# Performance work log

Measured on AMD Instinct MI355X. Metric: run time of the kernel, lower is better.

## Reference

```python
import jax, jax.numpy as jnp
import numpy as np

EPS = 1e-8
COMMITMENT_COST = 0.25
NUM_EMBEDDINGS = 8192
EMBEDDING_DIM = 256


def setup_inputs() -> dict:
    key = jax.random.key(0)
    k1, k2 = jax.random.split(key)
    z = jax.random.normal(k1, (4, 4096, EMBEDDING_DIM), dtype=jnp.float32)
    # nn.Embedding init: uniform(-1/K, 1/K)
    lim = 1.0 / NUM_EMBEDDINGS
    codebook = jax.random.uniform(k2, (NUM_EMBEDDINGS, EMBEDDING_DIM), dtype=jnp.float32,
                                  minval=-lim, maxval=lim)
    return {"z": z, "codebook": codebook}


def reference(z, codebook):
    input_shape = z.shape
    flat = z.reshape(-1, EMBEDDING_DIM)              # [N, D]
    # squared euclidean distances (argmin identical to cdist argmin)
    d2 = (jnp.sum(flat * flat, axis=1, keepdims=True)
          - 2.0 * flat @ codebook.T
          + jnp.sum(codebook * codebook, axis=1))    # [N, K]
    indices = jnp.argmin(d2, axis=1)                 # [N]
    c_star = codebook[indices]                       # [N, D] gather
    d_vec = c_star - flat
    # eval mode: v_d = d_vec (no noise)
    magnitude = jnp.linalg.norm(d_vec, axis=1, keepdims=True)          # [N, 1]
    direction = jax.lax.stop_gradient(
        d_vec / (jnp.linalg.norm(d_vec, axis=1, keepdims=True) + EPS))  # [N, D]
    z_q = (flat + magnitude * direction).reshape(input_shape)
    codebook_loss = jnp.mean((c_star - jax.lax.stop_gradient(flat)) ** 2)
    commitment_loss = jnp.mean((flat - jax.lax.stop_gradient(c_star)) ** 2)
    loss = codebook_loss + COMMITMENT_COST * commitment_loss
    return z_q, loss, indices.reshape(input_shape[:-1])
```

## Files before the change

### kernel.cpp

```cpp
#include <hip/hip_runtime.h>
#include <math.h>

#define NROWS 16384
#define KC 8192
#define DD 256
#define CAP 128
#define MARGIN 3.0e-4f

typedef __attribute__((ext_vector_type(8))) short bf16x8;
typedef __attribute__((ext_vector_type(4))) float f32x4;

__device__ __forceinline__ unsigned short f2bf(float f) {
    unsigned int u = __float_as_uint(f);
    unsigned int r = (u + 0x7FFFu + ((u >> 16) & 1u)) >> 16;
    return (unsigned short)r;
}
__device__ __forceinline__ unsigned int fenc(float f) {
    unsigned int u = __float_as_uint(f);
    return (u & 0x80000000u) ? ~u : (u | 0x80000000u);
}
__device__ __forceinline__ float fdec(unsigned int u) {
    return __uint_as_float((u & 0x80000000u) ? (u & 0x7FFFFFFFu) : ~u);
}

__device__ __forceinline__ float exact_d2(const float* __restrict__ zrow,
                                          const float* __restrict__ crow,
                                          float A, float C)
{
    float dot = 0.0f;
#pragma unroll 16
    for (int d = 0; d < DD; ++d) dot = fmaf(zrow[d], crow[d], dot);
    return __fadd_rn(__fsub_rn(A, 2.0f * dot), C);
}

__global__ __launch_bounds__(256)
void vq_prep(const float* __restrict__ z, const float* __restrict__ cb,
             unsigned short* __restrict__ zb, unsigned short* __restrict__ cbb,
             float* __restrict__ cc, float* __restrict__ rowA,
             int* __restrict__ cnt, unsigned int* __restrict__ rmin,
             float* __restrict__ loss_ptr)
{
    const int t = threadIdx.x;
    const int b = blockIdx.x;
    const size_t i = (size_t)b * 256 + t;
    {
        const float* src; unsigned short* dst; size_t off;
        if (i < 1048576) { src = z;  dst = zb;  off = i; }
        else             { src = cb; dst = cbb; off = i - 1048576; }
        float4 v = *(const float4*)(src + off * 4);
        ushort4 o;
        o.x = f2bf(v.x); o.y = f2bf(v.y); o.z = f2bf(v.z); o.w = f2bf(v.w);
        *(ushort4*)(dst + off * 4) = o;
    }
    if (b < 1536) {
        const int unit = b * 16 + (t >> 4);
        const int l = t & 15;
        const float* p = (unit < KC) ? (cb + (size_t)unit * DD)
                                     : (z + (size_t)(unit - KC) * DD);
        const float* q = p + 128 * (l >> 3) + (l & 7);
        float x0 = q[0];
        float r = __fmul_rn(x0, x0);
#pragma unroll
        for (int k = 1; k < 16; ++k) {
            const float x = q[8 * k];
            r = __fadd_rn(r, __fmul_rn(x, x));
        }
        r = __fadd_rn(r, __shfl_xor(r, 1, 64));
        r = __fadd_rn(r, __shfl_xor(r, 2, 64));
        r = __fadd_rn(r, __shfl_xor(r, 4, 64));
        r = __fadd_rn(r, __shfl_xor(r, 8, 64));
        if (l == 0) {
            if (unit < KC) cc[unit] = r;
            else rowA[unit - KC] = r;
        }
    } else if (b < 1664) {
        const int u = (b - 1536) * 256 + t;
        if (u < NROWS) cnt[u] = 0;
        else rmin[u - NROWS] = 0xFFFFFFFFu;
    }
    if (i == 0) *loss_ptr = 0.0f;
}

__global__ __launch_bounds__(256, 2)
void vq_gemm_screen(const unsigned short* __restrict__ cbb,
                    const unsigned short* __restrict__ zb,
                    const float* __restrict__ cc,
                    unsigned int* __restrict__ rowmin_u,
                    int* __restrict__ cnt, int* __restrict__ cand)
{
    __shared__ char Als[16384];
    __shared__ char Bls[16384];
    __shared__ float ccs[128];
    __shared__ float colmin_lds[2][128];
    __shared__ float thr_lds[128];

    const int t = threadIdx.x;
    const int lane = t & 63;
    const int w = t >> 6;
    const int cw = w >> 1;
    const int rw = w & 1;
    const int gr = blockIdx.x;
    const int gc = blockIdx.y;

    const char* gA = (const char*)(cbb + (size_t)gc * 128 * DD);
    const char* gB = (const char*)(zb  + (size_t)gr * 128 * DD);

    if (t < 128) ccs[t] = cc[gc * 128 + t];

    f32x4 acc[4][4];
#pragma unroll
    for (int i = 0; i < 4; ++i)
#pragma unroll
        for (int j = 0; j < 4; ++j) acc[i][j] = (f32x4)0.0f;

    const int rA = lane & 15;
    const int kq = (lane >> 4) * 16;

    for (int kc = 0; kc < 4; ++kc) {
        __syncthreads();
        {
            const int o0 = t * 16;
#pragma unroll
            for (int i = 0; i < 4; ++i) {
                const int o = i * 4096 + o0;
                const int row = o >> 7;
                const int col = (o & 127) ^ ((row & 7) << 4);
                const int gofs = row * 512 + kc * 128 + col;
                __builtin_amdgcn_global_load_lds(
                    (const unsigned int*)(gA + gofs),
                    (unsigned int*)(Als + i * 4096 + w * 1024), 16, 0, 0);
                __builtin_amdgcn_global_load_lds(
                    (const unsigned int*)(gB + gofs),
                    (unsigned int*)(Bls + i * 4096 + w * 1024), 16, 0, 0);
            }
        }
        __syncthreads();
#pragma unroll
        for (int ks = 0; ks < 2; ++ks) {
            bf16x8 af[4], bfr[4];
#pragma unroll
            for (int i = 0; i < 4; ++i) {
                const int c = cw * 64 + i * 16 + rA;
                af[i] = *(const bf16x8*)(Als + c * 128 +
                         ((ks * 64 + kq) ^ ((c & 7) << 4)));
                const int r = rw * 64 + i * 16 + rA;
                bfr[i] = *(const bf16x8*)(Bls + r * 128 +
                          ((ks * 64 + kq) ^ ((r & 7) << 4)));
            }
#pragma unroll
            for (int i = 0; i < 4; ++i)
#pragma unroll
                for (int j = 0; j < 4; ++j)
                    acc[i][j] = __builtin_amdgcn_mfma_f32_16x16x32_bf16(
                        af[i], bfr[j], acc[i][j], 0, 0, 0);
        }
    }

    const int lr = lane >> 4;
    float mj[4];
#pragma unroll
    for (int j = 0; j < 4; ++j) mj[j] = 3.0e38f;
#pragma unroll
    for (int i = 0; i < 4; ++i) {
#pragma unroll
        for (int r = 0; r < 4; ++r) {
            const float ccv = ccs[cw * 64 + i * 16 + lr * 4 + r];
#pragma unroll
            for (int j = 0; j < 4; ++j) {
                const float d = fmaf(-2.0f, acc[i][j][r], ccv);
                acc[i][j][r] = d;
                mj[j] = fminf(mj[j], d);
            }
        }
    }
#pragma unroll
    for (int j = 0; j < 4; ++j) {
        mj[j] = fminf(mj[j], __shfl_xor(mj[j], 16, 64));
        mj[j] = fminf(mj[j], __shfl_xor(mj[j], 32, 64));
        colmin_lds[cw][rw * 64 + j * 16 + (lane & 15)] = mj[j];
    }
    __syncthreads();

    if (t < 128) {
        const float cm = fminf(colmin_lds[0][t], colmin_lds[1][t]);
        const unsigned int enc = fenc(cm);
        const unsigned int old = atomicMin(&rowmin_u[gr * 128 + t], enc);
        const unsigned int cur = (old < enc) ? old : enc;
        thr_lds[t] = fdec(cur) + MARGIN;
    }
    __syncthreads();

#pragma unroll
    for (int j = 0; j < 4; ++j) {
        const int colL = rw * 64 + j * 16 + (lane & 15);
        const float thr = thr_lds[colL];
        const int rowg = gr * 128 + colL;
#pragma unroll
        for (int i = 0; i < 4; ++i)
#pragma unroll
            for (int r = 0; r < 4; ++r)
                if (acc[i][j][r] <= thr) {
                    const int pos = atomicAdd(&cnt[rowg], 1);
                    if (pos < CAP)
                        cand[(size_t)rowg * CAP + pos] =
                            gc * 128 + cw * 64 + i * 16 + lr * 4 + r;
                }
    }
}

__global__ __launch_bounds__(256)
void vq_finalize_out(const float* __restrict__ z, const float* __restrict__ cb,
                     const float* __restrict__ rowA, const float* __restrict__ cc,
                     const int* __restrict__ cnt, const int* __restrict__ cand,
                     float* __restrict__ zq, float* __restrict__ loss_ptr,
                     float* __restrict__ idx_out)
{
    __shared__ float wsum[4];
    const int t = threadIdx.x;
    const int lane = t & 63;
    const int w = t >> 6;
    const int row = blockIdx.x * 4 + w;
    const int n = cnt[row];
    const float A = rowA[row];
    const float* zrow = z + (size_t)row * DD;

    float best = 3.0e38f;
    int bidx = 0x7FFFFFFF;
    if (n <= CAP) {
        for (int base = 0; base < n; base += 64) {
            const int ci = base + lane;
            float d2 = 3.0e38f;
            int code = 0x7FFFFFFF;
            if (ci < n) {
                code = cand[(size_t)row * CAP + ci];
                d2 = exact_d2(zrow, cb + (size_t)code * DD, A, cc[code]);
            }
            if (d2 < best || (d2 == best && code < bidx)) { best = d2; bidx = code; }
        }
    } else {
        for (int code = lane; code < KC; code += 64) {
            const float d2 = exact_d2(zrow, cb + (size_t)code * DD, A, cc[code]);
            if (d2 < best || (d2 == best && code < bidx)) { best = d2; bidx = code; }
        }
    }
#pragma unroll
    for (int m = 1; m < 64; m <<= 1) {
        const float ov = __shfl_xor(best, m, 64);
        const int oi = __shfl_xor(bidx, m, 64);
        if (ov < best || (ov == best && oi < bidx)) { best = ov; bidx = oi; }
    }

    const int k = bidx;
    const float4 z4 = *(const float4*)(zrow + lane * 4);
    const float4 c4 = *(const float4*)(cb + (size_t)k * DD + lane * 4);
    float4 d4 = make_float4(c4.x - z4.x, c4.y - z4.y, c4.z - z4.z, c4.w - z4.w);
    float ss = fmaf(d4.x, d4.x, fmaf(d4.y, d4.y, fmaf(d4.z, d4.z, d4.w * d4.w)));
#pragma unroll
    for (int m = 1; m < 64; m <<= 1) ss += __shfl_xor(ss, m, 64);
    const float mag = sqrtf(ss);
    const float scale = mag / (mag + 1e-8f);
    float4 q = make_float4(fmaf(scale, d4.x, z4.x), fmaf(scale, d4.y, z4.y),
                           fmaf(scale, d4.z, z4.z), fmaf(scale, d4.w, z4.w));
    *(float4*)(zq + (size_t)row * DD + lane * 4) = q;
    if (lane == 0) {
        wsum[w] = ss;
        idx_out[row] = (float)k;
    }
    __syncthreads();
    if (t == 0) {
        const float s = (wsum[0] + wsum[1]) + (wsum[2] + wsum[3]);
        atomicAdd(loss_ptr, s * (1.25f / 4194304.0f));
    }
}

extern "C" void kernel_launch(void* const* d_in, const int* in_sizes, int n_in,
                              void* d_out, int out_size, void* d_ws, size_t ws_size,
                              hipStream_t stream)
{
    (void)in_sizes; (void)n_in; (void)out_size; (void)ws_size;
    const float* z = (const float*)d_in[0];
    const float* cb = (const float*)d_in[1];
    float* out = (float*)d_out;
    float* zq = out;
    float* loss_ptr = out + (size_t)NROWS * DD;
    float* idx_out = loss_ptr + 1;

    char* ws = (char*)d_ws;
    unsigned short* zb   = (unsigned short*)(ws);
    unsigned short* cbb  = (unsigned short*)(ws + 8388608);
    int*            cand = (int*)(ws + 12582912);
    int*            cnt  = (int*)(ws + 20971520);
    unsigned int*   rmin = (unsigned int*)(ws + 21037056);
    float*          cc   = (float*)(ws + 21102592);
    float*          rowA = (float*)(ws + 21135360);

    vq_prep<<<6144, 256, 0, stream>>>(z, cb, zb, cbb, cc, rowA, cnt, rmin, loss_ptr);
    vq_gemm_screen<<<dim3(NROWS / 128, KC / 128), 256, 0, stream>>>(
        cbb, zb, cc, rmin, cnt, cand);
    vq_finalize_out<<<NROWS / 4, 256, 0, stream>>>(
        z, cb, rowA, cc, cnt, cand, zq, loss_ptr, idx_out);
}
```

Baseline: 267.0 us.

## Enlarge GEMM screen tile to 256 rows and skip rescoring single candidates

The screening GEMM now covers 256 z rows per block instead of 128. Each wave holds a 4x8 grid of MFMA accumulators, which raises arithmetic intensity and halves the codebook tile reloads across the grid. This costs twice the accumulator registers and more LDS, so occupancy may drop under the 2-blocks launch bound. In finalize, rows with exactly one surviving candidate take it directly and skip the exact distance evaluation and wave reduction.

After: 288.2 us. 1.08x slower.

```diff
diff --git a/kernel.cpp b/kernel.cpp
--- a/kernel.cpp
+++ b/kernel.cpp
@@ -89,10 +89,10 @@
                     int* __restrict__ cnt, int* __restrict__ cand)
 {
     __shared__ char Als[16384];
-    __shared__ char Bls[16384];
+    __shared__ char Bls[32768];
     __shared__ float ccs[128];
-    __shared__ float colmin_lds[2][128];
-    __shared__ float thr_lds[128];
+    __shared__ float colmin_lds[2][256];
+    __shared__ float thr_lds[256];
 
     const int t = threadIdx.x;
     const int lane = t & 63;
@@ -103,70 +103,75 @@
     const int gc = blockIdx.y;
 
     const char* gA = (const char*)(cbb + (size_t)gc * 128 * DD);
-    const char* gB = (const char*)(zb  + (size_t)gr * 128 * DD);
+    const char* gB = (const char*)(zb  + (size_t)gr * 256 * DD);
 
     if (t < 128) ccs[t] = cc[gc * 128 + t];
 
-    f32x4 acc[4][4];
+    f32x4 acc[4][8];
 #pragma unroll
     for (int i = 0; i < 4; ++i)
 #pragma unroll
-        for (int j = 0; j < 4; ++j) acc[i][j] = (f32x4)0.0f;
+        for (int j = 0; j < 8; ++j) acc[i][j] = (f32x4)0.0f;
 
     const int rA = lane & 15;
     const int kq = (lane >> 4) * 16;
 
     for (int kc = 0; kc < 4; ++kc) {
         __syncthreads();
-        {
-            const int o0 = t * 16;
-#pragma unroll
-            for (int i = 0; i < 4; ++i) {
-                const int o = i * 4096 + o0;
-                const int row = o >> 7;
-                const int col = (o & 127) ^ ((row & 7) << 4);
-                const int gofs = row * 512 + kc * 128 + col;
-                __builtin_amdgcn_global_load_lds(
-                    (const unsigned int*)(gA + gofs),
-                    (unsigned int*)(Als + i * 4096 + w * 1024), 16, 0, 0);
-                __builtin_amdgcn_global_load_lds(
-                    (const unsigned int*)(gB + gofs),
-                    (unsigned int*)(Bls + i * 4096 + w * 1024), 16, 0, 0);
-            }
+#pragma unroll
+        for (int i = 0; i < 4; ++i) {
+            const int o = (i * 4 + w) * 1024 + lane * 16;
+            const int row = o >> 7;
+            const int col = (o & 127) ^ ((row & 7) << 4);
+            __builtin_amdgcn_global_load_lds(
+                (const unsigned int*)(gA + row * 512 + kc * 128 + col),
+                (unsigned int*)(Als + (i * 4 + w) * 1024), 16, 0, 0);
+        }
+#pragma unroll
+        for (int i = 0; i < 8; ++i) {
+            const int o = (i * 4 + w) * 1024 + lane * 16;
+            const int row = o >> 7;
+            const int col = (o & 127) ^ ((row & 7) << 4);
+            __builtin_amdgcn_global_load_lds(
+                (const unsigned int*)(gB + row * 512 + kc * 128 + col),
+                (unsigned int*)(Bls + (i * 4 + w) * 1024), 16, 0, 0);
         }
         __syncthreads();
 #pragma unroll
         for (int ks = 0; ks < 2; ++ks) {
-            bf16x8 af[4], bfr[4];
+            bf16x8 af[4], bfr[8];
 #pragma unroll
             for (int i = 0; i < 4; ++i) {
                 const int c = cw * 64 + i * 16 + rA;
                 af[i] = *(const bf16x8*)(Als + c * 128 +
                          ((ks * 64 + kq) ^ ((c & 7) << 4)));
-                const int r = rw * 64 + i * 16 + rA;
-                bfr[i] = *(const bf16x8*)(Bls + r * 128 +
+            }
+#pragma unroll
+            for (int j = 0; j < 8; ++j) {
+                const int r = rw * 128 + j * 16 + rA;
+                bfr[j] = *(const bf16x8*)(Bls + r * 128 +
                           ((ks * 64 + kq) ^ ((r & 7) << 4)));
             }
 #pragma unroll
             for (int i = 0; i < 4; ++i)
 #pragma unroll
-                for (int j = 0; j < 4; ++j)
+                for (int j = 0; j < 8; ++j)
                     acc[i][j] = __builtin_amdgcn_mfma_f32_16x16x32_bf16(
                         af[i], bfr[j], acc[i][j], 0, 0, 0);
         }
     }
 
     const int lr = lane >> 4;
-    float mj[4];
-#pragma unroll
-    for (int j = 0; j < 4; ++j) mj[j] = 3.0e38f;
+    float mj[8];
+#pragma unroll
+    for (int j = 0; j < 8; ++j) mj[j] = 3.0e38f;
 #pragma unroll
     for (int i = 0; i < 4; ++i) {
 #pragma unroll
         for (int r = 0; r < 4; ++r) {
             const float ccv = ccs[cw * 64 + i * 16 + lr * 4 + r];
 #pragma unroll
-            for (int j = 0; j < 4; ++j) {
+            for (int j = 0; j < 8; ++j) {
                 const float d = fmaf(-2.0f, acc[i][j][r], ccv);
                 acc[i][j][r] = d;
                 mj[j] = fminf(mj[j], d);
@@ -174,27 +179,27 @@
         }
     }
 #pragma unroll
-    for (int j = 0; j < 4; ++j) {
+    for (int j = 0; j < 8; ++j) {
         mj[j] = fminf(mj[j], __shfl_xor(mj[j], 16, 64));
         mj[j] = fminf(mj[j], __shfl_xor(mj[j], 32, 64));
-        colmin_lds[cw][rw * 64 + j * 16 + (lane & 15)] = mj[j];
+        colmin_lds[cw][rw * 128 + j * 16 + rA] = mj[j];
     }
     __syncthreads();
 
-    if (t < 128) {
+    {
         const float cm = fminf(colmin_lds[0][t], colmin_lds[1][t]);
         const unsigned int enc = fenc(cm);
-        const unsigned int old = atomicMin(&rowmin_u[gr * 128 + t], enc);
+        const unsigned int old = atomicMin(&rowmin_u[gr * 256 + t], enc);
         const unsigned int cur = (old < enc) ? old : enc;
         thr_lds[t] = fdec(cur) + MARGIN;
     }
     __syncthreads();
 
 #pragma unroll
-    for (int j = 0; j < 4; ++j) {
-        const int colL = rw * 64 + j * 16 + (lane & 15);
+    for (int j = 0; j < 8; ++j) {
+        const int colL = rw * 128 + j * 16 + rA;
         const float thr = thr_lds[colL];
-        const int rowg = gr * 128 + colL;
+        const int rowg = gr * 256 + colL;
 #pragma unroll
         for (int i = 0; i < 4; ++i)
 #pragma unroll
@@ -221,33 +226,38 @@
     const int w = t >> 6;
     const int row = blockIdx.x * 4 + w;
     const int n = cnt[row];
-    const float A = rowA[row];
     const float* zrow = z + (size_t)row * DD;
 
-    float best = 3.0e38f;
-    int bidx = 0x7FFFFFFF;
-    if (n <= CAP) {
-        for (int base = 0; base < n; base += 64) {
-            const int ci = base + lane;
-            float d2 = 3.0e38f;
-            int code = 0x7FFFFFFF;
-            if (ci < n) {
-                code = cand[(size_t)row * CAP + ci];
-                d2 = exact_d2(zrow, cb + (size_t)code * DD, A, cc[code]);
-            }
-            if (d2 < best || (d2 == best && code < bidx)) { best = d2; bidx = code; }
-        }
+    int bidx;
+    if (n == 1) {
+        bidx = cand[(size_t)row * CAP];
     } else {
-        for (int code = lane; code < KC; code += 64) {
-            const float d2 = exact_d2(zrow, cb + (size_t)code * DD, A, cc[code]);
-            if (d2 < best || (d2 == best && code < bidx)) { best = d2; bidx = code; }
-        }
-    }
-#pragma unroll
-    for (int m = 1; m < 64; m <<= 1) {
-        const float ov = __shfl_xor(best, m, 64);
-        const int oi = __shfl_xor(bidx, m, 64);
-        if (ov < best || (ov == best && oi < bidx)) { best = ov; bidx = oi; }
+        const float A = rowA[row];
+        float best = 3.0e38f;
+        bidx = 0x7FFFFFFF;
+        if (n <= CAP) {
+            for (int base = 0; base < n; base += 64) {
+                const int ci = base + lane;
+                float d2 = 3.0e38f;
+                int code = 0x7FFFFFFF;
+                if (ci < n) {
+                    code = cand[(size_t)row * CAP + ci];
+                    d2 = exact_d2(zrow, cb + (size_t)code * DD, A, cc[code]);
+                }
+                if (d2 < best || (d2 == best && code < bidx)) { best = d2; bidx = code; }
+            }
+        } else {
+            for (int code = lane; code < KC; code += 64) {
+                const float d2 = exact_d2(zrow, cb + (size_t)code * DD, A, cc[code]);
+                if (d2 < best || (d2 == best && code < bidx)) { best = d2; bidx = code; }
+            }
+        }
+#pragma unroll
+        for (int m = 1; m < 64; m <<= 1) {
+            const float ov = __shfl_xor(best, m, 64);
+            const int oi = __shfl_xor(bidx, m, 64);
+            if (ov < best || (ov == best && oi < bidx)) { best = ov; bidx = oi; }
+        }
     }
 
     const int k = bidx;
@@ -295,7 +305,7 @@
     float*          rowA = (float*)(ws + 21135360);
 
     vq_prep<<<6144, 256, 0, stream>>>(z, cb, zb, cbb, cc, rowA, cnt, rmin, loss_ptr);
-    vq_gemm_screen<<<dim3(NROWS / 128, KC / 128), 256, 0, stream>>>(
+    vq_gemm_screen<<<dim3(NROWS / 256, KC / 128), 256, 0, stream>>>(
         cbb, zb, cc, rmin, cnt, cand);
     vq_finalize_out<<<NROWS / 4, 256, 0, stream>>>(
         z, cb, rowA, cc, cnt, cand, zq, loss_ptr, idx_out);
```
